# Performance work log

Hardware: AMD Instinct MI355X
Metric: run time of the kernel (lower is better)

Reference implementation:

```python
import jax, jax.numpy as jnp
import numpy as np

NUM_HEADS = 16
EPS = 1e-6
ROPE_THETA = 10000.0


def _rmsnorm_fp32(x, w):
    # RMSNorm computed in fp32, scale by learned weight (per head_dim)
    xf = x.astype(jnp.float32)
    var = jnp.mean(xf * xf, axis=-1, keepdims=True)
    return (xf * jax.lax.rsqrt(var + EPS) * w.astype(jnp.float32)).astype(x.dtype)


def _rope_3d_angles(T, H, W, head_dim):
    # split head_dim across (t,h,w) axes; all parts even
    dh = 2 * ((head_dim // 3) // 2)
    dw = dh
    dt = head_dim - dh - dw

    def axis_ang(L, d):
        inv = 1.0 / (ROPE_THETA ** (jnp.arange(0, d, 2, dtype=jnp.float32) / d))
        return jnp.arange(L, dtype=jnp.float32)[:, None] * inv[None, :]  # [L, d//2]

    at = axis_ang(T, dt)  # [T, dt/2]
    ah = axis_ang(H, dh)  # [H, dh/2]
    aw = axis_ang(W, dw)  # [W, dw/2]
    # broadcast to [T,H,W, head_dim//2] then flatten to [N, head_dim//2]
    at_g = jnp.broadcast_to(at[:, None, None, :], (T, H, W, dt // 2))
    ah_g = jnp.broadcast_to(ah[None, :, None, :], (T, H, W, dh // 2))
    aw_g = jnp.broadcast_to(aw[None, None, :, :], (T, H, W, dw // 2))
    ang = jnp.concatenate([at_g, ah_g, aw_g], axis=-1).reshape(T * H * W, head_dim // 2)
    return jnp.cos(ang), jnp.sin(ang)


def _apply_rope(x, cos, sin):
    # x: [B,Hh,N,D]; cos/sin: [N, D/2]; interleaved complex-pair rotation
    xr = x[..., 0::2]
    xi = x[..., 1::2]
    c = cos[None, None, :, :]
    s = sin[None, None, :, :]
    out_r = xr * c - xi * s
    out_i = xr * s + xi * c
    return jnp.stack([out_r, out_i], axis=-1).reshape(x.shape)


def setup_inputs() -> dict:
    key = jax.random.key(0)
    ks = jax.random.split(key, 7)
    dim, hd = 2048, 128
    x = jax.random.normal(ks[0], (1, 2048, dim), dtype=jnp.float32)
    qkv_w = jax.random.normal(ks[1], (3 * dim, dim), dtype=jnp.float32) * (dim ** -0.5)
    qkv_b = jax.random.normal(ks[2], (3 * dim,), dtype=jnp.float32) * 0.02
    proj_w = jax.random.normal(ks[3], (dim, dim), dtype=jnp.float32) * (dim ** -0.5)
    proj_b = jax.random.normal(ks[4], (dim,), dtype=jnp.float32) * 0.02
    q_norm_w = jnp.ones((hd,), dtype=jnp.float32)
    k_norm_w = jnp.ones((hd,), dtype=jnp.float32)
    return {"x": x, "qkv_w": qkv_w, "qkv_b": qkv_b, "proj_w": proj_w,
            "proj_b": proj_b, "q_norm_w": q_norm_w, "k_norm_w": k_norm_w,
            "t_dim": 8, "h_dim": 16, "w_dim": 16}


def reference(x, qkv_w, qkv_b, proj_w, proj_b, q_norm_w, k_norm_w, t_dim, h_dim, w_dim):
    B, N, C = x.shape
    Hh = NUM_HEADS
    D = C // Hh
    scale = D ** -0.5
    # QKV projection (torch Linear: x @ W.T + b)
    qkv = x @ qkv_w.T + qkv_b                      # [B,N,3C]
    qkv = qkv.reshape(B, N, 3, Hh, D).transpose(2, 0, 3, 1, 4)  # [3,B,Hh,N,D]
    q, k, v = qkv[0], qkv[1], qkv[2]
    q = _rmsnorm_fp32(q, q_norm_w)
    k = _rmsnorm_fp32(k, k_norm_w)
    cos, sin = _rope_3d_angles(t_dim, h_dim, w_dim, D)
    q = _apply_rope(q, cos, sin)
    k = _apply_rope(k, cos, sin)
    # SDPA (non-causal)
    scores = jnp.einsum('bhqd,bhkd->bhqk', q, k) * scale
    attn = jax.nn.softmax(scores, axis=-1)
    out = jnp.einsum('bhqk,bhkd->bhqd', attn, v)   # [B,Hh,N,D]
    out = out.transpose(0, 2, 1, 3).reshape(B, N, C)
    return out @ proj_w.T + proj_b
```

## Files before the change

### kernel.cpp

```cpp
#include <hip/hip_runtime.h>
#include <hip/hip_bf16.h>
#include <cstdint>
#include <cstddef>

typedef __attribute__((ext_vector_type(8))) short bf16x8;
typedef __attribute__((ext_vector_type(4))) float f32x4;
typedef __attribute__((ext_vector_type(16))) float f32x16;

#define AS1 __attribute__((address_space(1)))
#define AS3 __attribute__((address_space(3)))

__device__ __forceinline__ void gload_lds16(const void* g, void* l) {
  __builtin_amdgcn_global_load_lds((const AS1 void*)g, (AS3 void*)l, 16, 0, 0);
}

__device__ __forceinline__ unsigned short f2bf(float x) {
  __hip_bfloat16 h = __float2bfloat16(x);
  return __builtin_bit_cast(unsigned short, h);
}
__device__ __forceinline__ float bf2f(unsigned short u) {
  return __builtin_bit_cast(float, (unsigned int)u << 16);
}
__device__ __forceinline__ unsigned cvtpk(float a, float b) {
  unsigned r;
  asm("v_cvt_pk_bf16_f32 %0, %1, %2" : "=v"(r) : "v"(a), "v"(b));
  return r;
}
__device__ __forceinline__ void pswap(unsigned& x, unsigned& y) {
  asm volatile("v_permlane32_swap_b32 %0, %1" : "+v"(x), "+v"(y));
}

__global__ __launch_bounds__(256) void k_cvt_bf16(const float* __restrict__ in,
                                                  unsigned short* __restrict__ out,
                                                  int n4) {
  int i = blockIdx.x * 256 + threadIdx.x;
  const int stride = gridDim.x * 256;
  for (; i < n4; i += stride) {
    float4 v = reinterpret_cast<const float4*>(in)[i];
    ushort4 o;
    o.x = f2bf(v.x); o.y = f2bf(v.y); o.z = f2bf(v.z); o.w = f2bf(v.w);
    reinterpret_cast<ushort4*>(out)[i] = o;
  }
}

__global__ __launch_bounds__(256) void k_rope_tab(float* __restrict__ cosT,
                                                  float* __restrict__ sinT,
                                                  const int* __restrict__ hdim,
                                                  const int* __restrict__ wdim) {
  int idx = blockIdx.x * 256 + threadIdx.x;
  if (idx >= 2048 * 64) return;
  const int n = idx >> 6, j = idx & 63;
  const int H = *hdim, W = *wdim;
  const int w = n % W;
  const int rem = n / W;
  const int h = rem % H;
  const int t = rem / H;
  float pos, i2, d;
  if (j < 22)      { pos = (float)t; i2 = (float)(2 * j);        d = 44.f; }
  else if (j < 43) { pos = (float)h; i2 = (float)(2 * (j - 22)); d = 42.f; }
  else             { pos = (float)w; i2 = (float)(2 * (j - 43)); d = 42.f; }
  const float ang = pos * powf(10000.0f, -i2 / d);
  cosT[idx] = cosf(ang);
  sinT[idx] = sinf(ang);
}

__global__ __launch_bounds__(256, 2) void k_gemmQKV(const unsigned short* __restrict__ A,
                                                    const unsigned short* __restrict__ B,
                                                    const float* __restrict__ bias,
                                                    unsigned short* __restrict__ C,
                                                    int M, int N, int K) {
  __shared__ __align__(16) char lds[81920];
  const int tid = threadIdx.x;
  const int lane = tid & 63;
  const int wid = tid >> 6;
  const int wr = wid >> 1, wc = wid & 1;

  const int xcd = blockIdx.x & 7;
  const int t = blockIdx.x >> 3;
  const int bx = xcd * 4 + (t & 3);
  const int by = t >> 2;
  const int row0 = by * 128, col0 = bx * 192;
  const int NT = K >> 6;

  auto stageA = [&](int grow0, int kcol0, char* slot) {
#pragma unroll
    for (int r = 0; r < 2; ++r) {
      const int off = r * 4096 + tid * 16;
      const int pair = off >> 7;
      const int un = (off & 127) ^ ((pair & 7) << 4);
      const int grow = pair * 2 + (un >> 6);
      gload_lds16(A + (size_t)(grow0 + grow) * K + kcol0 + ((un & 63) >> 1),
                  slot + r * 4096 + wid * 1024);
    }
  };
  auto stageB = [&](int grow0, int kcol0, char* slot) {
#pragma unroll
    for (int r = 0; r < 3; ++r) {
      const int off = r * 4096 + tid * 16;
      const int pair = off >> 7;
      const int un = (off & 127) ^ ((pair & 7) << 4);
      const int grow = pair * 2 + (un >> 6);
      gload_lds16(B + (size_t)(grow0 + grow) * K + kcol0 + ((un & 63) >> 1),
                  slot + r * 4096 + wid * 1024);
    }
  };
  auto frag = [&](const char* slot, int r, int kb) -> bf16x8 {
    return *reinterpret_cast<const bf16x8*>(
        slot + (r >> 1) * 128 + ((((r & 1) << 6) + kb) ^ (((r >> 1) & 7) << 4)));
  };

  f32x4 acc[4][6];
#pragma unroll
  for (int i = 0; i < 4; ++i)
#pragma unroll
    for (int j = 0; j < 6; ++j) acc[i][j] = (f32x4){0.f, 0.f, 0.f, 0.f};

  stageA(row0, 0,  lds);
  stageB(col0, 0,  lds + 16384);
  stageA(row0, 32, lds + 8192);
  stageB(col0, 32, lds + 28672);
  asm volatile("s_waitcnt vmcnt(5)" ::: "memory");
  __builtin_amdgcn_s_barrier();

  const int kb = (lane >> 4) << 4;
  for (int j = 0; j < NT; ++j) {
    const int b = j & 1, bp = b ^ 1;
    const char* base = lds + b * 40960;
    char* pbase = lds + bp * 40960;
    const bool pf = (j + 1 < NT);
    const int kn = (j + 1) * 64;
    bf16x8 af[4], bq[6];

#pragma unroll
    for (int fr = 0; fr < 4; ++fr) af[fr] = frag(base, wr * 64 + fr * 16 + (lane & 15), kb);
#pragma unroll
    for (int fc = 0; fc < 6; ++fc) bq[fc] = frag(base + 16384, wc * 96 + fc * 16 + (lane & 15), kb);
    if (pf) { stageA(row0, kn, pbase); stageB(col0, kn, pbase + 16384); }
    if (pf) asm volatile("s_waitcnt vmcnt(5)" ::: "memory");
    else    asm volatile("s_waitcnt vmcnt(0)" ::: "memory");
    __builtin_amdgcn_s_barrier();
    __builtin_amdgcn_s_setprio(1);
#pragma unroll
    for (int fr = 0; fr < 4; ++fr)
#pragma unroll
      for (int fc = 0; fc < 6; ++fc)
        acc[fr][fc] = __builtin_amdgcn_mfma_f32_16x16x32_bf16(af[fr], bq[fc], acc[fr][fc], 0, 0, 0);
    __builtin_amdgcn_s_setprio(0);
    __builtin_amdgcn_s_barrier();

#pragma unroll
    for (int fr = 0; fr < 4; ++fr) af[fr] = frag(base + 8192, wr * 64 + fr * 16 + (lane & 15), kb);
#pragma unroll
    for (int fc = 0; fc < 6; ++fc) bq[fc] = frag(base + 28672, wc * 96 + fc * 16 + (lane & 15), kb);
    if (pf) { stageA(row0, kn + 32, pbase + 8192); stageB(col0, kn + 32, pbase + 28672); }
    if (pf) asm volatile("s_waitcnt vmcnt(5)" ::: "memory");
    __builtin_amdgcn_s_barrier();
    __builtin_amdgcn_s_setprio(1);
#pragma unroll
    for (int fr = 0; fr < 4; ++fr)
#pragma unroll
      for (int fc = 0; fc < 6; ++fc)
        acc[fr][fc] = __builtin_amdgcn_mfma_f32_16x16x32_bf16(af[fr], bq[fc], acc[fr][fc], 0, 0, 0);
    __builtin_amdgcn_s_setprio(0);
    __builtin_amdgcn_s_barrier();
  }

#pragma unroll
  for (int fr = 0; fr < 4; ++fr)
#pragma unroll
    for (int fc = 0; fc < 6; ++fc) {
      const int col = col0 + wc * 96 + fc * 16 + (lane & 15);
      const float bv = bias[col];
#pragma unroll
      for (int jj = 0; jj < 4; ++jj) {
        const int row = row0 + wr * 64 + fr * 16 + (lane >> 4) * 4 + jj;
        C[(size_t)row * N + col] = f2bf(acc[fr][fc][jj] + bv);
      }
    }
}

__global__ __launch_bounds__(256) void k_gemm_bt_sk(const unsigned short* __restrict__ A,
                                                    const unsigned short* __restrict__ B,
                                                    float* __restrict__ Cp,
                                                    int M, int N, int K, int KS) {
  __shared__ __align__(16) unsigned short As[128 * 32];
  __shared__ __align__(16) unsigned short Bs[128 * 32];
  const int lane = threadIdx.x & 63;
  const int wid  = threadIdx.x >> 6;
  const int wr = wid >> 1, wc = wid & 1;
  const int rowA0 = blockIdx.y * 128;
  const int rowB0 = blockIdx.x * 128;
  const int k0 = blockIdx.z * KS;

  f32x4 acc[4][4];
#pragma unroll
  for (int i = 0; i < 4; ++i)
#pragma unroll
    for (int j = 0; j < 4; ++j) acc[i][j] = (f32x4){0.f, 0.f, 0.f, 0.f};

  for (int kt = k0; kt < k0 + KS; kt += 32) {
#pragma unroll
    for (int i = 0; i < 2; ++i) {
      const int c = i * 4 + wid;
      const int off = c * 1024 + lane * 16;
      const int row = off >> 6;
      const int col = (off & 63) >> 1;
      gload_lds16(A + (size_t)(rowA0 + row) * K + kt + col, (char*)As + c * 1024);
      gload_lds16(B + (size_t)(rowB0 + row) * K + kt + col, (char*)Bs + c * 1024);
    }
    __syncthreads();
    bf16x8 af[4], bfr[4];
#pragma unroll
    for (int mi = 0; mi < 4; ++mi)
      af[mi] = *reinterpret_cast<const bf16x8*>(
          &As[(wr * 64 + mi * 16 + (lane & 15)) * 32 + (lane >> 4) * 8]);
#pragma unroll
    for (int ni = 0; ni < 4; ++ni)
      bfr[ni] = *reinterpret_cast<const bf16x8*>(
          &Bs[(wc * 64 + ni * 16 + (lane & 15)) * 32 + (lane >> 4) * 8]);
#pragma unroll
    for (int mi = 0; mi < 4; ++mi)
#pragma unroll
      for (int ni = 0; ni < 4; ++ni)
        acc[mi][ni] = __builtin_amdgcn_mfma_f32_16x16x32_bf16(af[mi], bfr[ni], acc[mi][ni], 0, 0, 0);
    __syncthreads();
  }

  float* Cz = Cp + (size_t)blockIdx.z * M * N;
#pragma unroll
  for (int mi = 0; mi < 4; ++mi)
#pragma unroll
    for (int ni = 0; ni < 4; ++ni) {
      const int col = rowB0 + wc * 64 + ni * 16 + (lane & 15);
#pragma unroll
      for (int j = 0; j < 4; ++j) {
        const int row = rowA0 + wr * 64 + mi * 16 + (lane >> 4) * 4 + j;
        Cz[(size_t)row * N + col] = acc[mi][ni][j];
      }
    }
}

__global__ __launch_bounds__(256) void k_addbias(const float* __restrict__ Cp,
                                                 const float* __restrict__ bias,
                                                 float* __restrict__ out) {
  const int i = blockIdx.x * 256 + threadIdx.x;
  const float4 a = reinterpret_cast<const float4*>(Cp)[i];
  const float4 b = reinterpret_cast<const float4*>(Cp + 2048ull * 2048)[i];
  const float4 bv = reinterpret_cast<const float4*>(bias)[i & 511];
  float4 o;
  o.x = a.x + b.x + bv.x; o.y = a.y + b.y + bv.y;
  o.z = a.z + b.z + bv.z; o.w = a.w + b.w + bv.w;
  reinterpret_cast<float4*>(out)[i] = o;
}

__global__ __launch_bounds__(256) void k_qk_post(const unsigned short* __restrict__ qkv,
                                                 const float* __restrict__ qw,
                                                 const float* __restrict__ kw,
                                                 const float* __restrict__ cosT,
                                                 const float* __restrict__ sinT,
                                                 unsigned short* __restrict__ qo,
                                                 unsigned short* __restrict__ ko) {
  const int lane = threadIdx.x & 63;
  const int wid = threadIdx.x >> 6;
  const int pair = blockIdx.x * 4 + wid;
  const int n = pair >> 4, h = pair & 15;
  const float c = cosT[n * 64 + lane];
  const float s = sinT[n * 64 + lane];
#pragma unroll
  for (int sq = 0; sq < 2; ++sq) {
    const unsigned short* src = qkv + (size_t)n * 6144 + sq * 2048 + h * 128;
    const unsigned int vp = reinterpret_cast<const unsigned int*>(src)[lane];
    const float vx = bf2f((unsigned short)(vp & 0xffff));
    const float vy = bf2f((unsigned short)(vp >> 16));
    float ss = vx * vx + vy * vy;
#pragma unroll
    for (int m = 1; m < 64; m <<= 1) ss += __shfl_xor(ss, m, 64);
    const float r = rsqrtf(ss * (1.0f / 128.0f) + 1e-6f);
    float2 wv = reinterpret_cast<const float2*>(sq == 0 ? qw : kw)[lane];
    const float xr = vx * r * wv.x;
    const float xi = vy * r * wv.y;
    float orr = xr * c - xi * s;
    float oi  = xr * s + xi * c;
    if (sq == 0) { orr *= 0.08838834764831845f; oi *= 0.08838834764831845f; }
    unsigned short* dst = (sq == 0 ? qo : ko) + ((size_t)h * 2048 + n) * 128 + 2 * lane;
    const unsigned int pk = (unsigned int)f2bf(orr) | ((unsigned int)f2bf(oi) << 16);
    *reinterpret_cast<unsigned int*>(dst) = pk;
  }
}

__global__ __launch_bounds__(256) void k_v_tr(const unsigned short* __restrict__ qkv,
                                              unsigned short* __restrict__ vt2) {
  __shared__ __align__(16) unsigned short tile[64][136];
  const int h = blockIdx.y;
  const int n0 = blockIdx.x * 64;
  const int t = threadIdx.x;
  {
    const int row = t >> 2;
    const int c0 = (t & 3) * 32;
    const unsigned short* src = qkv + (size_t)(n0 + row) * 6144 + 4096 + h * 128 + c0;
#pragma unroll
    for (int j = 0; j < 32; j += 8)
      *reinterpret_cast<bf16x8*>(&tile[row][c0 + j]) =
          *reinterpret_cast<const bf16x8*>(src + j);
  }
  __syncthreads();
#pragma unroll
  for (int g4 = 0; g4 < 4; ++g4) {
    const int g = g4 * 256 + t;
    const int c = g >> 8;
    const int dblk = (g >> 6) & 3;
    const int p = g & 63;
    const int d = dblk * 32 + (p & 31);
    const int hi = p >> 5;
    bf16x8 o;
#pragma unroll
    for (int e = 0; e < 8; ++e) o[e] = (short)tile[c * 16 + hi * 8 + e][d];
    const size_t oidx = ((((size_t)h * 128 + (n0 >> 4) + c) * 4 + dblk) * 64 + p) * 8;
    *reinterpret_cast<bf16x8*>(vt2 + oidx) = o;
  }
}

__global__ __launch_bounds__(256) void k_fattn(const unsigned short* __restrict__ q,
                                               const unsigned short* __restrict__ k,
                                               const unsigned short* __restrict__ vt2,
                                               unsigned short* __restrict__ Onorm,
                                               float* __restrict__ lseb) {
  __shared__ __align__(16) unsigned short Ks[2][64 * 128];
  __shared__ __align__(16) unsigned short Vs[2][64 * 128];
  const int lane = threadIdx.x & 63;
  const int wid = threadIdx.x >> 6;
  const int hi2 = lane >> 5;
  const int ql = lane & 31;
  const int bid = blockIdx.x;
  const int h = bid & 15;
  const int qb = (bid >> 4) & 15;
  const int ksp = bid >> 8;
  const int q0 = qb * 128 + wid * 32;
  const int kbase = ksp * 1024;

  auto stageK = [&](int buf, int kt2) {
#pragma unroll
    for (int r = 0; r < 4; ++r) {
      const int off = r * 4096 + (wid * 64 + lane) * 16;
      const int row = off >> 8;
      const int colb = (off & 255) ^ ((row & 15) << 4);
      gload_lds16(k + ((size_t)h * 2048 + kbase + kt2 * 64 + row) * 128 + (colb >> 1),
                  (char*)Ks[buf] + r * 4096 + wid * 1024);
    }
  };
  auto stageV = [&](int buf, int kt2) {
    const unsigned short* vbase = vt2 + ((size_t)h * 128 + (kbase >> 4) + kt2 * 4) * 2048;
#pragma unroll
    for (int r = 0; r < 4; ++r)
      gload_lds16(vbase + r * 2048 + (wid * 64 + lane) * 8,
                  (char*)Vs[buf] + r * 4096 + wid * 1024);
  };

  bf16x8 qf[8];
  {
    const unsigned short* qp = q + ((size_t)h * 2048 + q0 + ql) * 128 + hi2 * 8;
#pragma unroll
    for (int c = 0; c < 8; ++c) qf[c] = *reinterpret_cast<const bf16x8*>(qp + c * 16);
  }
  f32x16 O[4];
#pragma unroll
  for (int i = 0; i < 4; ++i)
#pragma unroll
    for (int j = 0; j < 16; ++j) O[i][j] = 0.f;
  float m = -1e30f, l = 0.f;

  stageK(0, 0);
  stageV(0, 0);
  asm volatile("s_waitcnt vmcnt(0)" ::: "memory");
  __builtin_amdgcn_s_barrier();

  const int kswz = (lane & 15) << 4;
  for (int kt = 0; kt < 16; ++kt) {
    const int cur = kt & 1;
    const bool pf = (kt + 1 < 16);
    if (pf) { stageK(cur ^ 1, kt + 1); stageV(cur ^ 1, kt + 1); }

    f32x16 s0, s1;
#pragma unroll
    for (int j = 0; j < 16; ++j) { s0[j] = 0.f; s1[j] = 0.f; }
    __builtin_amdgcn_s_setprio(1);
#pragma unroll
    for (int c = 0; c < 8; ++c) {
      bf16x8 a0 = *reinterpret_cast<const bf16x8*>(
          (const char*)Ks[cur] + ql * 256 + ((c * 32 + hi2 * 16) ^ kswz));
      s0 = __builtin_amdgcn_mfma_f32_32x32x16_bf16(a0, qf[c], s0, 0, 0, 0);
    }
#pragma unroll
    for (int c = 0; c < 8; ++c) {
      bf16x8 a1 = *reinterpret_cast<const bf16x8*>(
          (const char*)Ks[cur] + (32 + ql) * 256 + ((c * 32 + hi2 * 16) ^ kswz));
      s1 = __builtin_amdgcn_mfma_f32_32x32x16_bf16(a1, qf[c], s1, 0, 0, 0);
    }
    __builtin_amdgcn_s_setprio(0);

    float mt = s0[0];
#pragma unroll
    for (int j = 1; j < 16; ++j) mt = fmaxf(mt, s0[j]);
#pragma unroll
    for (int j = 0; j < 16; ++j) mt = fmaxf(mt, s1[j]);
    mt = fmaxf(mt, __shfl_xor(mt, 32, 64));

    if (!__all(mt <= m + 8.0f)) {
      const float mn = fmaxf(m, mt);
      const float al = __expf(m - mn);
      m = mn;
      l *= al;
#pragma unroll
      for (int i = 0; i < 4; ++i)
#pragma unroll
        for (int j = 0; j < 16; ++j) O[i][j] *= al;
    }
    float rs = 0.f;
#pragma unroll
    for (int j = 0; j < 16; ++j) {
      s0[j] = __expf(s0[j] - m); rs += s0[j];
      s1[j] = __expf(s1[j] - m); rs += s1[j];
    }
    rs += __shfl_xor(rs, 32, 64);
    l += rs;

    bf16x8 pfr[4];
#pragma unroll
    for (int half = 0; half < 2; ++half) {
      const f32x16& sv = half ? s1 : s0;
      unsigned a[8];
#pragma unroll
      for (int j2 = 0; j2 < 8; ++j2) a[j2] = cvtpk(sv[2 * j2], sv[2 * j2 + 1]);
      pswap(a[0], a[2]);
      pswap(a[1], a[3]);
      pswap(a[4], a[6]);
      pswap(a[5], a[7]);
      union { uint4 u; bf16x8 v; } p0, p1;
      p0.u.x = a[0]; p0.u.y = a[1]; p0.u.z = a[2]; p0.u.w = a[3];
      p1.u.x = a[4]; p1.u.y = a[5]; p1.u.z = a[6]; p1.u.w = a[7];
      pfr[half * 2 + 0] = p0.v;
      pfr[half * 2 + 1] = p1.v;
    }

    __builtin_amdgcn_s_setprio(1);
#pragma unroll
    for (int dblk = 0; dblk < 4; ++dblk) {
#pragma unroll
      for (int c2 = 0; c2 < 4; ++c2) {
        bf16x8 va = *reinterpret_cast<const bf16x8*>(
            (const char*)Vs[cur] + ((c2 * 4 + dblk) * 64 + lane) * 16);
        O[dblk] = __builtin_amdgcn_mfma_f32_32x32x16_bf16(va, pfr[c2], O[dblk], 0, 0, 0);
      }
    }
    __builtin_amdgcn_s_setprio(0);

    if (pf) {
      asm volatile("s_waitcnt vmcnt(0)" ::: "memory");
      __builtin_amdgcn_s_barrier();
    }
  }

  const float rl = 1.0f / l;
  const int n = q0 + ql;
  unsigned short* ob = Onorm + (((size_t)(ksp * 16 + h) * 2048) + n) * 128;
#pragma unroll
  for (int dblk = 0; dblk < 4; ++dblk)
#pragma unroll
    for (int a = 0; a < 4; ++a) {
      uint2 w;
      w.x = (unsigned)f2bf(O[dblk][a * 4 + 0] * rl) | ((unsigned)f2bf(O[dblk][a * 4 + 1] * rl) << 16);
      w.y = (unsigned)f2bf(O[dblk][a * 4 + 2] * rl) | ((unsigned)f2bf(O[dblk][a * 4 + 3] * rl) << 16);
      *reinterpret_cast<uint2*>(ob + dblk * 32 + a * 8 + hi2 * 4) = w;
    }
  if (hi2 == 0)
    lseb[(size_t)(ksp * 16 + h) * 2048 + n] = m + logf(l);
}

__global__ __launch_bounds__(256) void k_merge(const unsigned short* __restrict__ Onorm,
                                               const float* __restrict__ lseb,
                                               unsigned short* __restrict__ att) {
  const int idx = blockIdx.x * 256 + threadIdx.x;
  const int n = idx >> 8;
  const int r = idx & 255;
  const int h = r >> 4;
  const int d0 = (r & 15) * 8;
  const float l0 = lseb[(size_t)h * 2048 + n];
  const float l1 = lseb[(size_t)(16 + h) * 2048 + n];
  const float M = fmaxf(l0, l1);
  float w0 = __expf(l0 - M), w1 = __expf(l1 - M);
  const float inv = 1.0f / (w0 + w1);
  w0 *= inv; w1 *= inv;
  const bf16x8 o0 = *reinterpret_cast<const bf16x8*>(
      Onorm + ((size_t)h * 2048 + n) * 128 + d0);
  const bf16x8 o1 = *reinterpret_cast<const bf16x8*>(
      Onorm + ((size_t)(16 + h) * 2048 + n) * 128 + d0);
  bf16x8 o;
#pragma unroll
  for (int e = 0; e < 8; ++e)
    o[e] = (short)f2bf(bf2f((unsigned short)o0[e]) * w0 + bf2f((unsigned short)o1[e]) * w1);
  *reinterpret_cast<bf16x8*>(att + (size_t)n * 2048 + h * 128 + d0) = o;
}

extern "C" void kernel_launch(void* const* d_in, const int* in_sizes, int n_in,
                              void* d_out, int out_size, void* d_ws, size_t ws_size,
                              hipStream_t stream) {
  (void)in_sizes; (void)n_in; (void)out_size; (void)ws_size;
  const float* x      = (const float*)d_in[0];
  const float* qkv_w  = (const float*)d_in[1];
  const float* qkv_b  = (const float*)d_in[2];
  const float* proj_w = (const float*)d_in[3];
  const float* proj_b = (const float*)d_in[4];
  const float* q_nw   = (const float*)d_in[5];
  const float* k_nw   = (const float*)d_in[6];
  const int* h_dim    = (const int*)d_in[8];
  const int* w_dim    = (const int*)d_in[9];
  float* out = (float*)d_out;

  char* ws = (char*)d_ws;
  size_t off = 0;
  auto carve = [&](size_t bytes) -> void* {
    void* p = ws + off;
    off += (bytes + 255) & ~(size_t)255;
    return p;
  };
  unsigned short* x_bf   = (unsigned short*)carve(2048ull * 2048 * 2);
  unsigned short* w1_bf  = (unsigned short*)carve(6144ull * 2048 * 2);
  unsigned short* w2_bf  = (unsigned short*)carve(2048ull * 2048 * 2);
  unsigned short* qkvb   = (unsigned short*)carve(2048ull * 6144 * 2);
  unsigned short* q_bf   = (unsigned short*)carve(16ull * 2048 * 128 * 2);
  unsigned short* k_bf   = (unsigned short*)carve(16ull * 2048 * 128 * 2);
  unsigned short* vt2_bf = (unsigned short*)carve(16ull * 2048 * 128 * 2);
  unsigned short* att_bf = (unsigned short*)carve(2048ull * 2048 * 2);
  unsigned short* on_bf  = (unsigned short*)carve(2ull * 16 * 2048 * 128 * 2);
  float*          lseb   = (float*)carve(2ull * 16 * 2048 * 4);
  float*          projp  = (float*)carve(2ull * 2048 * 2048 * 4);
  float*          cosT   = (float*)carve(2048ull * 64 * 4);
  float*          sinT   = (float*)carve(2048ull * 64 * 4);

  hipLaunchKernelGGL(k_cvt_bf16, dim3(2048), dim3(256), 0, stream, x, x_bf, 2048 * 2048 / 4);
  hipLaunchKernelGGL(k_cvt_bf16, dim3(2048), dim3(256), 0, stream, qkv_w, w1_bf, 6144 * 2048 / 4);
  hipLaunchKernelGGL(k_cvt_bf16, dim3(2048), dim3(256), 0, stream, proj_w, w2_bf, 2048 * 2048 / 4);
  hipLaunchKernelGGL(k_rope_tab, dim3(512), dim3(256), 0, stream, cosT, sinT, h_dim, w_dim);
  hipLaunchKernelGGL(k_gemmQKV, dim3(512), dim3(256), 0, stream,
                     x_bf, w1_bf, qkv_b, qkvb, 2048, 6144, 2048);
  hipLaunchKernelGGL(k_qk_post, dim3(8192), dim3(256), 0, stream,
                     qkvb, q_nw, k_nw, cosT, sinT, q_bf, k_bf);
  hipLaunchKernelGGL(k_v_tr, dim3(32, 16), dim3(256), 0, stream, qkvb, vt2_bf);
  hipLaunchKernelGGL(k_fattn, dim3(512), dim3(256), 0, stream,
                     q_bf, k_bf, vt2_bf, on_bf, lseb);
  hipLaunchKernelGGL(k_merge, dim3(2048), dim3(256), 0, stream, on_bf, lseb, att_bf);
  hipLaunchKernelGGL(k_gemm_bt_sk, dim3(16, 16, 2), dim3(256), 0, stream,
                     att_bf, w2_bf, projp, 2048, 2048, 2048, 1024);
  hipLaunchKernelGGL(k_addbias, dim3(4096), dim3(256), 0, stream, projp, proj_b, out);
}
```

Baseline: 186.3 us.

## Pipeline projection GEMM with double-buffered swizzled LDS and drop trailing barriers

Replaces the simple split-K projection GEMM, which loaded one 32-wide K slice and synchronized twice per step, with a double-buffered 64-wide K pipeline. It uses XOR-swizzled LDS layout and async global-to-LDS prefetch overlapped with MFMA. It also removes the trailing barrier after each MFMA phase in both this and the QKV GEMM, relying on the next phase's barrier. The aim is to hide global load latency and cut LDS bank conflicts and sync overhead. The cost is 64KB of LDS per block, which may limit occupancy, plus a risk of races from the removed barriers.

```diff
diff --git a/kernel.cpp b/kernel.cpp
--- a/kernel.cpp
+++ b/kernel.cpp
@@ -146,7 +146,6 @@
       for (int fc = 0; fc < 6; ++fc)
         acc[fr][fc] = __builtin_amdgcn_mfma_f32_16x16x32_bf16(af[fr], bq[fc], acc[fr][fc], 0, 0, 0);
     __builtin_amdgcn_s_setprio(0);
-    __builtin_amdgcn_s_barrier();
 
 #pragma unroll
     for (int fr = 0; fr < 4; ++fr) af[fr] = frag(base + 8192, wr * 64 + fr * 16 + (lane & 15), kb);
@@ -162,7 +161,6 @@
       for (int fc = 0; fc < 6; ++fc)
         acc[fr][fc] = __builtin_amdgcn_mfma_f32_16x16x32_bf16(af[fr], bq[fc], acc[fr][fc], 0, 0, 0);
     __builtin_amdgcn_s_setprio(0);
-    __builtin_amdgcn_s_barrier();
   }
 
 #pragma unroll
@@ -179,18 +177,35 @@
     }
 }
 
-__global__ __launch_bounds__(256) void k_gemm_bt_sk(const unsigned short* __restrict__ A,
-                                                    const unsigned short* __restrict__ B,
-                                                    float* __restrict__ Cp,
-                                                    int M, int N, int K, int KS) {
-  __shared__ __align__(16) unsigned short As[128 * 32];
-  __shared__ __align__(16) unsigned short Bs[128 * 32];
-  const int lane = threadIdx.x & 63;
-  const int wid  = threadIdx.x >> 6;
+__global__ __launch_bounds__(256, 2) void k_gemmProj(const unsigned short* __restrict__ A,
+                                                     const unsigned short* __restrict__ B,
+                                                     float* __restrict__ Cp,
+                                                     int M, int N, int K, int KS) {
+  __shared__ __align__(16) char lds[65536];
+  const int tid = threadIdx.x;
+  const int lane = tid & 63;
+  const int wid = tid >> 6;
   const int wr = wid >> 1, wc = wid & 1;
-  const int rowA0 = blockIdx.y * 128;
-  const int rowB0 = blockIdx.x * 128;
+  const int row0 = blockIdx.y * 128;
+  const int col0 = blockIdx.x * 128;
   const int k0 = blockIdx.z * KS;
+  const int NT = KS >> 6;
+
+  auto stageS = [&](const unsigned short* src, int grow0, int kcol0, char* slot) {
+#pragma unroll
+    for (int r = 0; r < 2; ++r) {
+      const int off = r * 4096 + tid * 16;
+      const int pair = off >> 7;
+      const int un = (off & 127) ^ ((pair & 7) << 4);
+      const int grow = pair * 2 + (un >> 6);
+      gload_lds16(src + (size_t)(grow0 + grow) * K + kcol0 + ((un & 63) >> 1),
+                  slot + r * 4096 + wid * 1024);
+    }
+  };
+  auto frag = [&](const char* slot, int r, int kb) -> bf16x8 {
+    return *reinterpret_cast<const bf16x8*>(
+        slot + (r >> 1) * 128 + ((((r & 1) << 6) + kb) ^ (((r >> 1) & 7) << 4)));
+  };
 
   f32x4 acc[4][4];
 #pragma unroll
@@ -198,44 +213,64 @@
 #pragma unroll
     for (int j = 0; j < 4; ++j) acc[i][j] = (f32x4){0.f, 0.f, 0.f, 0.f};
 
-  for (int kt = k0; kt < k0 + KS; kt += 32) {
-#pragma unroll
-    for (int i = 0; i < 2; ++i) {
-      const int c = i * 4 + wid;
-      const int off = c * 1024 + lane * 16;
-      const int row = off >> 6;
-      const int col = (off & 63) >> 1;
-      gload_lds16(A + (size_t)(rowA0 + row) * K + kt + col, (char*)As + c * 1024);
-      gload_lds16(B + (size_t)(rowB0 + row) * K + kt + col, (char*)Bs + c * 1024);
-    }
-    __syncthreads();
-    bf16x8 af[4], bfr[4];
-#pragma unroll
-    for (int mi = 0; mi < 4; ++mi)
-      af[mi] = *reinterpret_cast<const bf16x8*>(
-          &As[(wr * 64 + mi * 16 + (lane & 15)) * 32 + (lane >> 4) * 8]);
-#pragma unroll
-    for (int ni = 0; ni < 4; ++ni)
-      bfr[ni] = *reinterpret_cast<const bf16x8*>(
-          &Bs[(wc * 64 + ni * 16 + (lane & 15)) * 32 + (lane >> 4) * 8]);
-#pragma unroll
-    for (int mi = 0; mi < 4; ++mi)
-#pragma unroll
-      for (int ni = 0; ni < 4; ++ni)
-        acc[mi][ni] = __builtin_amdgcn_mfma_f32_16x16x32_bf16(af[mi], bfr[ni], acc[mi][ni], 0, 0, 0);
-    __syncthreads();
+  stageS(A, row0, k0,      lds);
+  stageS(B, col0, k0,      lds + 16384);
+  stageS(A, row0, k0 + 32, lds + 8192);
+  stageS(B, col0, k0 + 32, lds + 24576);
+  asm volatile("s_waitcnt vmcnt(4)" ::: "memory");
+  __builtin_amdgcn_s_barrier();
+
+  const int kb = (lane >> 4) << 4;
+  for (int j = 0; j < NT; ++j) {
+    const int b = j & 1, bp = b ^ 1;
+    const char* base = lds + b * 32768;
+    char* pbase = lds + bp * 32768;
+    const bool pf = (j + 1 < NT);
+    const int kn = k0 + (j + 1) * 64;
+    bf16x8 af[4], bq[4];
+
+#pragma unroll
+    for (int fr = 0; fr < 4; ++fr) af[fr] = frag(base, wr * 64 + fr * 16 + (lane & 15), kb);
+#pragma unroll
+    for (int fc = 0; fc < 4; ++fc) bq[fc] = frag(base + 16384, wc * 64 + fc * 16 + (lane & 15), kb);
+    if (pf) { stageS(A, row0, kn, pbase); stageS(B, col0, kn, pbase + 16384); }
+    if (pf) asm volatile("s_waitcnt vmcnt(4)" ::: "memory");
+    else    asm volatile("s_waitcnt vmcnt(0)" ::: "memory");
+    __builtin_amdgcn_s_barrier();
+    __builtin_amdgcn_s_setprio(1);
+#pragma unroll
+    for (int fr = 0; fr < 4; ++fr)
+#pragma unroll
+      for (int fc = 0; fc < 4; ++fc)
+        acc[fr][fc] = __builtin_amdgcn_mfma_f32_16x16x32_bf16(af[fr], bq[fc], acc[fr][fc], 0, 0, 0);
+    __builtin_amdgcn_s_setprio(0);
+
+#pragma unroll
+    for (int fr = 0; fr < 4; ++fr) af[fr] = frag(base + 8192, wr * 64 + fr * 16 + (lane & 15), kb);
+#pragma unroll
+    for (int fc = 0; fc < 4; ++fc) bq[fc] = frag(base + 24576, wc * 64 + fc * 16 + (lane & 15), kb);
+    if (pf) { stageS(A, row0, kn + 32, pbase + 8192); stageS(B, col0, kn + 32, pbase + 24576); }
+    if (pf) asm volatile("s_waitcnt vmcnt(4)" ::: "memory");
+    __builtin_amdgcn_s_barrier();
+    __builtin_amdgcn_s_setprio(1);
+#pragma unroll
+    for (int fr = 0; fr < 4; ++fr)
+#pragma unroll
+      for (int fc = 0; fc < 4; ++fc)
+        acc[fr][fc] = __builtin_amdgcn_mfma_f32_16x16x32_bf16(af[fr], bq[fc], acc[fr][fc], 0, 0, 0);
+    __builtin_amdgcn_s_setprio(0);
   }
 
   float* Cz = Cp + (size_t)blockIdx.z * M * N;
 #pragma unroll
-  for (int mi = 0; mi < 4; ++mi)
-#pragma unroll
-    for (int ni = 0; ni < 4; ++ni) {
-      const int col = rowB0 + wc * 64 + ni * 16 + (lane & 15);
-#pragma unroll
-      for (int j = 0; j < 4; ++j) {
-        const int row = rowA0 + wr * 64 + mi * 16 + (lane >> 4) * 4 + j;
-        Cz[(size_t)row * N + col] = acc[mi][ni][j];
+  for (int fr = 0; fr < 4; ++fr)
+#pragma unroll
+    for (int fc = 0; fc < 4; ++fc) {
+      const int col = col0 + wc * 64 + fc * 16 + (lane & 15);
+#pragma unroll
+      for (int jj = 0; jj < 4; ++jj) {
+        const int row = row0 + wr * 64 + fr * 16 + (lane >> 4) * 4 + jj;
+        Cz[(size_t)row * N + col] = acc[fr][fc][jj];
       }
     }
 }
@@ -549,7 +584,7 @@
   hipLaunchKernelGGL(k_fattn, dim3(512), dim3(256), 0, stream,
                      q_bf, k_bf, vt2_bf, on_bf, lseb);
   hipLaunchKernelGGL(k_merge, dim3(2048), dim3(256), 0, stream, on_bf, lseb, att_bf);
-  hipLaunchKernelGGL(k_gemm_bt_sk, dim3(16, 16, 2), dim3(256), 0, stream,
+  hipLaunchKernelGGL(k_gemmProj, dim3(16, 16, 2), dim3(256), 0, stream,
                      att_bf, w2_bf, projp, 2048, 2048, 2048, 1024);
   hipLaunchKernelGGL(k_addbias, dim3(4096), dim3(256), 0, stream, projp, proj_b, out);
 }
```

After: 177.6 us. -4.7%, faster.
